# Optimization experiments

Measured on AMD Instinct MI355X. Metric: run time of the kernel, lower is better.

## Reference

```python
import jax, jax.numpy as jnp
import numpy as np

H, D, RPE_DIM, LAYERS = 8, 64, 64, 3
B, N = 8, 4096
EPS = 1e-8


def _srms(x):
    # SimpleRMSNorm: x / (||x||_2 / sqrt(d) + eps) == x / (rms(x) + eps)
    rms = jnp.sqrt(jnp.mean(x * x, axis=-1, keepdims=True))
    return x / (rms + EPS)


def _rpe(pos, w_in, b_in, w_layers, b_layers, w_out, b_out):
    # pos: [nf, 1] -> [nf, H*2*D]
    x = pos @ w_in + b_in
    for i in range(LAYERS):  # fixed small layer count
        x = jax.nn.relu(_srms(x)) @ w_layers[i] + b_layers[i]
    return jax.nn.relu(_srms(x)) @ w_out + b_out


def setup_inputs() -> dict:
    key = jax.random.key(0)
    ks = jax.random.split(key, 4)
    s = 0.02
    return {
        "x": jax.random.normal(ks[0], (B, H, N, D), jnp.float32),
        "w_in": jax.random.normal(ks[1], (1, RPE_DIM), jnp.float32) * s,
        "b_in": jnp.zeros((RPE_DIM,), jnp.float32),
        "w_layers": jax.random.normal(ks[2], (LAYERS, RPE_DIM, RPE_DIM), jnp.float32) * s,
        "b_layers": jnp.zeros((LAYERS, RPE_DIM), jnp.float32),
        "w_out": jax.random.normal(ks[3], (RPE_DIM, H * 2 * D), jnp.float32) * s,
        "b_out": jnp.zeros((H * 2 * D,), jnp.float32),
    }


def reference(x, w_in, b_in, w_layers, b_layers, w_out, b_out):
    # x: [b, h, n, d]; non-causal TnoFD with act_type='none' (identity act_fun)
    n = x.shape[-2]
    fft_size = 2 * n
    nf = fft_size // 2 + 1  # n + 1 frequencies
    pos = jnp.linspace(0.0, np.pi, nf, dtype=x.dtype).reshape(nf, 1)
    res = _rpe(pos, w_in, b_in, w_layers, b_layers, w_out, b_out)  # [nf, H*2D]
    # rearrange 'n (h d) -> h n d'
    res = res.reshape(nf, H, 2 * D).transpose(1, 0, 2)  # [H, nf, 2D]
    real, imag = res[..., :D], res[..., D:]
    imag = imag.at[:, 0, :].set(0.0).at[:, -1, :].set(0.0)
    a = real + 1j * imag  # [H, nf, D] complex filter
    y = jnp.fft.rfft(x, n=fft_size, axis=-2)  # [b, H, nf, D]
    out = jnp.fft.irfft(a * y, n=fft_size, axis=-2)[:, :, :n, :]
    return out.astype(x.dtype)
```

## Files before the change

### kernel.cpp

```cpp
#include <hip/hip_runtime.h>
#include <math.h>


#define PI_F 3.14159265358979323846f
#define TWO_PI_F 6.283185307179586f

__device__ __forceinline__ int dr4_3(int k) {
    return ((k & 3) << 4) | (k & 12) | ((k >> 4) & 3);
}

__global__ __launch_bounds__(512) void gen_tw_kernel(float2* __restrict__ tw4096,
                                                     float2* __restrict__ tw8192,
                                                     float2* __restrict__ e64)
{
    int idx = blockIdx.x * 512 + threadIdx.x;
    if (idx < 4096) {
        float s, c; __sincosf(TWO_PI_F * (float)idx * (1.0f / 4096.0f), &s, &c);
        tw4096[idx] = make_float2(c, s);
    } else if (idx < 8192) {
        int j = idx - 4096;
        float s, c; __sincosf(TWO_PI_F * (float)j * (1.0f / 8192.0f), &s, &c);
        tw8192[j] = make_float2(c, s);
    } else if (idx < 8256) {
        int j = idx - 8192;
        float s, c; __sincosf(TWO_PI_F * (float)j * (1.0f / 64.0f), &s, &c);
        e64[j] = make_float2(c, s);
    }
}

__device__ __forceinline__ void fft64_dif(float* re, float* im, int col, int ncol,
                                          int w, int nw, float sgn, bool act,
                                          const float2* e64s) {
    for (int S = 16, st = 1; S >= 1; S >>= 2, st <<= 2) {
        if (act) {
            for (int j = w; j < 16; j += nw) {
                const int q = j & (S - 1);
                const int u = q * st;
                const int i0 = ((j & ~(S - 1)) << 2) | q;
                const int p0 = i0 * ncol + col, p1 = (i0 + S) * ncol + col;
                const int p2 = (i0 + 2 * S) * ncol + col, p3 = (i0 + 3 * S) * ncol + col;
                float x0r = re[p0], x0i = im[p0], x1r = re[p1], x1i = im[p1];
                float x2r = re[p2], x2i = im[p2], x3r = re[p3], x3i = im[p3];
                float A0r = x0r + x2r, A0i = x0i + x2i, A1r = x0r - x2r, A1i = x0i - x2i;
                float A2r = x1r + x3r, A2i = x1i + x3i, A3r = x1r - x3r, A3i = x1i - x3i;
                float2 t1 = e64s[u], t2 = e64s[2 * u], t3 = e64s[3 * u];
                float c1 = t1.x, s1 = sgn * t1.y;
                float c2 = t2.x, s2 = sgn * t2.y;
                float c3 = t3.x, s3 = sgn * t3.y;
                re[p0] = A0r + A2r; im[p0] = A0i + A2i;
                float t1r = A1r - sgn * A3i, t1i = A1i + sgn * A3r;
                re[p1] = t1r * c1 - t1i * s1; im[p1] = t1r * s1 + t1i * c1;
                float t2r = A0r - A2r, t2i = A0i - A2i;
                re[p2] = t2r * c2 - t2i * s2; im[p2] = t2r * s2 + t2i * c2;
                float t3r = A1r + sgn * A3i, t3i = A1i - sgn * A3r;
                re[p3] = t3r * c3 - t3i * s3; im[p3] = t3r * s3 + t3i * c3;
            }
        }
        __syncthreads();
    }
}

__device__ __forceinline__ void fft64_dit(float* re, float* im, int col, int ncol,
                                          int w, int nw, float sgn, bool act,
                                          const float2* e64s) {
    for (int S = 1, st = 16; S <= 16; S <<= 2, st >>= 2) {
        if (act) {
            for (int j = w; j < 16; j += nw) {
                const int q = j & (S - 1);
                const int u = q * st;
                const int i0 = ((j & ~(S - 1)) << 2) | q;
                const int p0 = i0 * ncol + col, p1 = (i0 + S) * ncol + col;
                const int p2 = (i0 + 2 * S) * ncol + col, p3 = (i0 + 3 * S) * ncol + col;
                float y0r = re[p0], y0i = im[p0], y1r = re[p1], y1i = im[p1];
                float y2r = re[p2], y2i = im[p2], y3r = re[p3], y3i = im[p3];
                float2 t1 = e64s[u], t2 = e64s[2 * u], t3 = e64s[3 * u];
                float c1 = t1.x, s1 = sgn * t1.y;
                float c2 = t2.x, s2 = sgn * t2.y;
                float c3 = t3.x, s3 = sgn * t3.y;
                float x1r = y1r * c1 - y1i * s1, x1i = y1r * s1 + y1i * c1;
                float x2r = y2r * c2 - y2i * s2, x2i = y2r * s2 + y2i * c2;
                float x3r = y3r * c3 - y3i * s3, x3i = y3r * s3 + y3i * c3;
                float B0r = y0r + x2r, B0i = y0i + x2i, B1r = y0r - x2r, B1i = y0i - x2i;
                float B2r = x1r + x3r, B2i = x1i + x3i, B3r = x1r - x3r, B3i = x1i - x3i;
                re[p0] = B0r + B2r; im[p0] = B0i + B2i;
                re[p1] = B1r - sgn * B3i; im[p1] = B1i + sgn * B3r;
                re[p2] = B0r - B2r; im[p2] = B0i - B2i;
                re[p3] = B1r + sgn * B3i; im[p3] = B1i - sgn * B3r;
            }
        }
        __syncthreads();
    }
}

__global__ __launch_bounds__(256) void mlp_hidden_kernel(
    const float* __restrict__ w_in, const float* __restrict__ b_in,
    const float* __restrict__ w_layers, const float* __restrict__ b_layers,
    float* __restrict__ rbuf)
{
    const int lane = threadIdx.x & 63;
    const int k = blockIdx.x * 4 + (threadIdx.x >> 6);
    if (k > 4096) return;
    const float pos = PI_F * (float)k * (1.0f / 4096.0f);
    float xv = fmaf(pos, w_in[lane], b_in[lane]);
    for (int l = 0; l < 3; ++l) {
        float ss = xv * xv;
        #pragma unroll
        for (int o = 1; o < 64; o <<= 1) ss += __shfl_xor(ss, o, 64);
        float r = xv / (sqrtf(ss * (1.0f / 64.0f)) + 1e-8f);
        r = fmaxf(r, 0.0f);
        const float* W = w_layers + l * 4096;
        float a0 = 0.f, a1 = 0.f, a2 = 0.f, a3 = 0.f;
        for (int i = 0; i < 64; i += 4) {
            a0 = fmaf(__shfl(r, i, 64),     W[(i) * 64 + lane],     a0);
            a1 = fmaf(__shfl(r, i + 1, 64), W[(i + 1) * 64 + lane], a1);
            a2 = fmaf(__shfl(r, i + 2, 64), W[(i + 2) * 64 + lane], a2);
            a3 = fmaf(__shfl(r, i + 3, 64), W[(i + 3) * 64 + lane], a3);
        }
        xv = ((a0 + a1) + (a2 + a3)) + b_layers[l * 64 + lane];
    }
    float ss = xv * xv;
    #pragma unroll
    for (int o = 1; o < 64; o <<= 1) ss += __shfl_xor(ss, o, 64);
    float r = xv / (sqrtf(ss * (1.0f / 64.0f)) + 1e-8f);
    r = fmaxf(r, 0.0f);
    rbuf[(size_t)k * 64 + lane] = r;
}

__global__ __launch_bounds__(256) void mlp_out_kernel(
    const float* __restrict__ rbuf, const float* __restrict__ w_out,
    const float* __restrict__ b_out, float* __restrict__ res)
{
    __shared__ float rl[16 * 64];
    const int tid = threadIdx.x;
    const int nt = blockIdx.x, kt = blockIdx.y;
    for (int it = 0; it < 4; ++it) {
        int idx = it * 256 + tid;
        int row = idx >> 6, i = idx & 63;
        int k = kt * 16 + row;
        rl[idx] = (k <= 4096) ? rbuf[(size_t)k * 64 + i] : 0.0f;
    }
    __syncthreads();
    const int n = nt * 256 + tid;
    float acc[16];
    #pragma unroll
    for (int j = 0; j < 16; ++j) acc[j] = 0.0f;
    for (int i = 0; i < 64; ++i) {
        float wv = w_out[(size_t)i * 1024 + n];
        #pragma unroll
        for (int j = 0; j < 16; ++j)
            acc[j] = fmaf(rl[j * 64 + i], wv, acc[j]);
    }
    float bv = b_out[n];
    for (int j = 0; j < 16; ++j) {
        int k = kt * 16 + j;
        if (k <= 4096) res[(size_t)k * 1024 + n] = acc[j] + bv;
    }
}

__global__ __launch_bounds__(256) void fwd1_kernel(const float* __restrict__ x,
                                                   float2* __restrict__ Y,
                                                   const float2* __restrict__ tw4096,
                                                   const float2* __restrict__ e64g,
                                                   int slab_base)
{
    __shared__ float re[4096], im[4096];
    __shared__ float2 e64s[64];
    __shared__ float2 twA[64];
    const int tid = threadIdx.x;
    const int m0 = blockIdx.x, lslab = blockIdx.y;
    if (tid < 64) e64s[tid] = e64g[tid];
    else if (tid < 128) twA[tid - 64] = tw4096[m0 * (tid - 64)];
    const float* xs = x + (size_t)(slab_base + lslab) * 262144;
    for (int it = 0; it < 16; ++it) {
        int flat = it * 256 + tid;
        int m1 = flat >> 7, rr = (flat >> 6) & 1, d = flat & 63;
        float v = xs[(size_t)(128 * m1 + 2 * m0 + rr) * 64 + d];
        if (rr == 0) re[m1 * 64 + d] = v; else im[m1 * 64 + d] = v;
    }
    for (int i = 2048 + tid; i < 4096; i += 256) { re[i] = 0.0f; im[i] = 0.0f; }
    __syncthreads();
    const int d = tid & 63, w = tid >> 6;
    fft64_dif(re, im, d, 64, w, 4, -1.0f, true, e64s);
    float2* Ys = Y + (size_t)lslab * 262144 + (size_t)m0 * 64;
    for (int og = 0; og < 16; ++og) {
        int k1 = og * 4 + w;
        int slot = dr4_3(k1);
        float vr = re[slot * 64 + d], vi = im[slot * 64 + d];
        float2 t = twA[k1];
        float c = t.x, s = -t.y;
        Ys[(size_t)k1 * 4096 + d] = make_float2(vr * c - vi * s, vr * s + vi * c);
    }
}

__global__ __launch_bounds__(512) void midspec_kernel(float2* __restrict__ Y,
                                                      const float* __restrict__ res,
                                                      const float2* __restrict__ tw4096,
                                                      const float2* __restrict__ tw8192,
                                                      const float2* __restrict__ e64g,
                                                      int slab_base)
{
    __shared__ float re[8192], im[8192];
    __shared__ float2 e64s[64];
    __shared__ float2 twS[64];
    __shared__ float2 twB[128];
    const int tid = threadIdx.x;
    const int k1p = blockIdx.x;
    const int lslab = blockIdx.y;
    const int h = (slab_base + lslab) & 7;
    const bool pairwg = (k1p >= 1 && k1p <= 31);
    const int k1a = k1p;
    const int k1b = pairwg ? (64 - k1p) : k1p;
    const int NC = pairwg ? 128 : 64;

    if (tid < 64) e64s[tid] = e64g[tid];
    else if (tid < 128) twS[tid - 64] = tw8192[(tid - 64) * 64 + k1a];
    else if (tid < 256) {
        int i = tid - 128;
        int kk1 = (i < 64) ? k1a : k1b;
        twB[i] = tw4096[(i & 63) * kk1];
    }

    const float2* Pa = Y + (size_t)lslab * 262144 + (size_t)k1a * 4096;
    for (int it = 0; it < 4; ++it) {
        int idx4 = it * 512 + tid;
        const float4 v = ((const float4*)Pa)[idx4];
        int lin = idx4 * 2, m0 = lin >> 6, d = lin & 63;
        re[m0 * 128 + d] = v.x;     im[m0 * 128 + d] = v.y;
        re[m0 * 128 + d + 1] = v.z; im[m0 * 128 + d + 1] = v.w;
    }
    if (pairwg) {
        const float2* Pb = Y + (size_t)lslab * 262144 + (size_t)k1b * 4096;
        for (int it = 0; it < 4; ++it) {
            int idx4 = it * 512 + tid;
            const float4 v = ((const float4*)Pb)[idx4];
            int lin = idx4 * 2, m0 = lin >> 6, d = lin & 63;
            re[m0 * 128 + 64 + d] = v.x;     im[m0 * 128 + 64 + d] = v.y;
            re[m0 * 128 + 64 + d + 1] = v.z; im[m0 * 128 + 64 + d + 1] = v.w;
        }
    }
    __syncthreads();
    const int col = tid & 127, w8 = tid >> 7;
    fft64_dif(re, im, col, 128, w8, 4, -1.0f, col < NC, e64s);

    const int nit = pairwg ? 8 : 4;
    for (int it = 0; it < nit; ++it) {
        int item = it * 512 + tid;
        int k0 = item >> 6, d = item & 63;
        int c = h * 128 + d;
        if (k1p == 0 && k0 == 0) {
            float C0r = re[d], C0i = im[d];
            float X0 = C0r + C0i, XN = C0r - C0i;
            float a0 = res[c], aN = res[(size_t)4096 * 1024 + c];
            float S0 = a0 * X0, SN = aN * XN;
            re[d] = 0.5f * (S0 + SN); im[d] = 0.5f * (S0 - SN);
            int p2 = 2 * 128 + d;
            float Cr = re[p2], Ci = im[p2];
            float ar = res[(size_t)2048 * 1024 + c], ai = res[(size_t)2048 * 1024 + c + 64];
            float Sr = ar * Cr + ai * Ci, Si = ai * Cr - ar * Ci;
            re[p2] = Sr; im[p2] = -Si;
        } else {
            int k0p, coff;
            if (pairwg)          { k0p = 63 - k0;        coff = 64; }
            else if (k1p == 0)   { k0p = (64 - k0) & 63; coff = 0;  }
            else  { k0p = 63 - k0;        coff = 0;  }
            int sa = dr4_3(k0)  * 128 + d;
            int sb = dr4_3(k0p) * 128 + coff + d;
            int k  = k0 * 64 + k1a;
            int km = 4096 - k;
            float Ckr = re[sa], Cki = im[sa];
            float Cmr = re[sb], Cmi = im[sb];
            float Er = 0.5f * (Ckr + Cmr), Ei = 0.5f * (Cki - Cmi);
            float Dr = 0.5f * (Ckr - Cmr), Di = 0.5f * (Cki + Cmi);
            float Or = Di, Oi = -Dr;
            float2 tk = twS[k0];
            float cw = tk.x, sw = -tk.y;
            float Tr = Or * cw - Oi * sw, Ti = Or * sw + Oi * cw;
            float Xkr = Er + Tr, Xki = Ei + Ti;
            float Xmr = Er - Tr, Xmi = Ti - Ei;
            float akr = res[(size_t)k * 1024 + c],  aki = res[(size_t)k * 1024 + c + 64];
            float amr = res[(size_t)km * 1024 + c], ami = res[(size_t)km * 1024 + c + 64];
            float Skr = akr * Xkr - aki * Xki, Ski = akr * Xki + aki * Xkr;
            float Smr = amr * Xmr - ami * Xmi, Smi = amr * Xmi + ami * Xmr;
            float Epr = 0.5f * (Skr + Smr), Epi = 0.5f * (Ski - Smi);
            float Ddr = 0.5f * (Skr - Smr), Ddi = 0.5f * (Ski + Smi);
            float Opr = Ddr * cw + Ddi * sw, Opi = Ddi * cw - Ddr * sw;
            re[sa] = Epr - Opi; im[sa] = Epi + Opr;
            re[sb] = Epr + Opi; im[sb] = Opr - Epi;
        }
    }
    __syncthreads();
    fft64_dit(re, im, col, 128, w8, 4, +1.0f, col < NC, e64s);

    const int nit2 = pairwg ? 16 : 8;
    for (int it = 0; it < nit2; ++it) {
        int item = it * 512 + tid;
        int pl = item >> 12, rem = item & 4095;
        int m0 = rem >> 6, d = rem & 63;
        int cc = pl * 64 + d;
        int k1 = pl ? k1b : k1a;
        float vr = re[m0 * 128 + cc], vi = im[m0 * 128 + cc];
        float2 t = twB[pl * 64 + m0];
        float c2 = t.x, s = t.y;
        Y[(size_t)lslab * 262144 + (size_t)k1 * 4096 + (size_t)m0 * 64 + d] =
            make_float2(vr * c2 - vi * s, vr * s + vi * c2);
    }
}

__global__ __launch_bounds__(256) void inv2_kernel(const float2* __restrict__ Y,
                                                   float* __restrict__ out,
                                                   const float2* __restrict__ e64g,
                                                   int slab_base)
{
    __shared__ float re[4096], im[4096];
    __shared__ float2 e64s[64];
    const int tid = threadIdx.x;
    const int m0 = blockIdx.x, lslab = blockIdx.y;
    if (tid < 64) e64s[tid] = e64g[tid];
    const float2* Ys = Y + (size_t)lslab * 262144 + (size_t)m0 * 64;
    for (int it = 0; it < 8; ++it) {
        int idx4 = it * 256 + tid;
        int lin = idx4 * 2, k1 = lin >> 6, d = lin & 63;
        const float4 v = ((const float4*)Ys)[k1 * 2048 + (d >> 1)];
        re[k1 * 64 + d] = v.x;     im[k1 * 64 + d] = v.y;
        re[k1 * 64 + d + 1] = v.z; im[k1 * 64 + d + 1] = v.w;
    }
    __syncthreads();
    const int d = tid & 63, w = tid >> 6;
    fft64_dif(re, im, d, 64, w, 4, +1.0f, true, e64s);
    float* os = out + (size_t)(slab_base + lslab) * 262144;
    const float sc = 1.0f / 4096.0f;
    for (int it = 0; it < 16; ++it) {
        int flat = it * 256 + tid;
        int m1 = flat >> 7, rr = (flat >> 6) & 1, dd = flat & 63;
        int slot = dr4_3(m1);
        float v = rr ? im[slot * 64 + dd] : re[slot * 64 + dd];
        os[(size_t)(128 * m1 + 2 * m0 + rr) * 64 + dd] = v * sc;
    }
}

#define PADF(i) ((i) + ((i) >> 5))

__device__ __forceinline__ unsigned dr4_12(unsigned k) {
    unsigned rb = __brev(k) >> 20;
    return ((rb & 0x555u) << 1) | ((rb >> 1) & 0x555u);
}

__global__ __launch_bounds__(64) void rpe_mlp_kernel(
    const float* __restrict__ w_in, const float* __restrict__ b_in,
    const float* __restrict__ w_layers, const float* __restrict__ b_layers,
    const float* __restrict__ w_out, const float* __restrict__ b_out,
    float* __restrict__ res)
{
    const int k = blockIdx.x;
    const int lane = threadIdx.x;
    const float pos = PI_F * (float)k * (1.0f / 4096.0f);
    float xv = fmaf(pos, w_in[lane], b_in[lane]);
    for (int l = 0; l < 3; ++l) {
        float ss = xv * xv;
        #pragma unroll
        for (int o = 1; o < 64; o <<= 1) ss += __shfl_xor(ss, o, 64);
        float rms = sqrtf(ss * (1.0f / 64.0f));
        float r = xv / (rms + 1e-8f);
        r = r > 0.0f ? r : 0.0f;
        const float* W = w_layers + l * 64 * 64;
        float acc = b_layers[l * 64 + lane];
        for (int i = 0; i < 64; ++i)
            acc = fmaf(__shfl(r, i, 64), W[i * 64 + lane], acc);
        xv = acc;
    }
    float ss = xv * xv;
    #pragma unroll
    for (int o = 1; o < 64; o <<= 1) ss += __shfl_xor(ss, o, 64);
    float rms = sqrtf(ss * (1.0f / 64.0f));
    float r = xv / (rms + 1e-8f);
    r = r > 0.0f ? r : 0.0f;
    float acc[16];
    #pragma unroll
    for (int u = 0; u < 16; ++u) acc[u] = b_out[u * 64 + lane];
    for (int i = 0; i < 64; ++i) {
        float rv = __shfl(r, i, 64);
        const float* Wrow = w_out + i * 1024;
        #pragma unroll
        for (int u = 0; u < 16; ++u)
            acc[u] = fmaf(rv, Wrow[u * 64 + lane], acc[u]);
    }
    float* dst = res + (size_t)k * 1024;
    #pragma unroll
    for (int u = 0; u < 16; ++u) dst[u * 64 + lane] = acc[u];
}

__global__ __launch_bounds__(256) void fftconv_kernel(
    const float* __restrict__ x, const float* __restrict__ res,
    float* __restrict__ out)
{
    __shared__ float re[PADF(4095) + 1];
    __shared__ float im[PADF(4095) + 1];
    const int tid = threadIdx.x;
    const int blk = blockIdx.x;
    const int d = (blk >> 3) & 63;
    const int slab = (blk & 7) | ((blk >> 9) << 3);
    const int h = slab & 7;
    const size_t base = (size_t)slab * 4096 * 64 + (size_t)d;
    const float* xc = x + base;
    float* oc = out + base;
    const int c = h * 128 + d;
    for (int m = tid; m < 2048; m += 256) {
        re[PADF(m)] = xc[(size_t)(2 * m) * 64];
        im[PADF(m)] = xc[(size_t)(2 * m + 1) * 64];
    }
    for (int m = 2048 + tid; m < 4096; m += 256) { re[PADF(m)] = 0.0f; im[PADF(m)] = 0.0f; }
    __syncthreads();
    for (int S = 1024; S >= 1; S >>= 2) {
        const float ab = -TWO_PI_F / (float)(4 * S);
        for (int j = tid; j < 1024; j += 256) {
            const int q = j & (S - 1);
            const int i0 = ((j & ~(S - 1)) << 2) | q;
            const int p0 = PADF(i0), p1 = PADF(i0 + S), p2 = PADF(i0 + 2 * S), p3 = PADF(i0 + 3 * S);
            float x0r = re[p0], x0i = im[p0], x1r = re[p1], x1i = im[p1];
            float x2r = re[p2], x2i = im[p2], x3r = re[p3], x3i = im[p3];
            float A0r = x0r + x2r, A0i = x0i + x2i, A1r = x0r - x2r, A1i = x0i - x2i;
            float A2r = x1r + x3r, A2i = x1i + x3i, A3r = x1r - x3r, A3i = x1i - x3i;
            float s1, c1; __sincosf(ab * (float)q, &s1, &c1);
            float c2 = c1 * c1 - s1 * s1, s2 = 2.0f * c1 * s1;
            float c3 = c2 * c1 - s2 * s1, s3 = s2 * c1 + c2 * s1;
            re[p0] = A0r + A2r; im[p0] = A0i + A2i;
            float t1r = A1r + A3i, t1i = A1i - A3r;
            re[p1] = t1r * c1 - t1i * s1; im[p1] = t1r * s1 + t1i * c1;
            float t2r = A0r - A2r, t2i = A0i - A2i;
            re[p2] = t2r * c2 - t2i * s2; im[p2] = t2r * s2 + t2i * c2;
            float t3r = A1r - A3i, t3i = A1i + A3r;
            re[p3] = t3r * c3 - t3i * s3; im[p3] = t3r * s3 + t3i * c3;
        }
        __syncthreads();
    }
    for (int k = tid; k <= 2048; k += 256) {
        if (k == 0) {
            float C0r = re[0], C0i = im[0];
            float X0 = C0r + C0i, XN = C0r - C0i;
            float a0 = res[c], aN = res[(size_t)4096 * 1024 + c];
            float S0 = a0 * X0, SN = aN * XN;
            re[0] = 0.5f * (S0 + SN); im[0] = 0.5f * (S0 - SN);
        } else if (k == 2048) {
            const int p = PADF(2);
            float Cr = re[p], Ci = im[p];
            float ar = res[(size_t)2048 * 1024 + c], ai = res[(size_t)2048 * 1024 + c + 64];
            float Sr = ar * Cr + ai * Ci, Si = ai * Cr - ar * Ci;
            re[p] = Sr; im[p] = -Si;
        } else {
            const int pk = PADF((int)dr4_12((unsigned)k));
            const int pm = PADF((int)dr4_12((unsigned)(4096 - k)));
            float Ckr = re[pk], Cki = im[pk];
            float Cmr = re[pm], Cmi = im[pm];
            float Er = 0.5f * (Ckr + Cmr), Ei = 0.5f * (Cki - Cmi);
            float Dr = 0.5f * (Ckr - Cmr), Di = 0.5f * (Cki + Cmi);
            float Or = Di, Oi = -Dr;
            float sw, cw; __sincosf(-TWO_PI_F * (float)k * (1.0f / 8192.0f), &sw, &cw);
            float Tr = Or * cw - Oi * sw, Ti = Or * sw + Oi * cw;
            float Xkr = Er + Tr, Xki = Ei + Ti;
            float Xmr = Er - Tr, Xmi = Ti - Ei;
            float akr = res[(size_t)k * 1024 + c], aki = res[(size_t)k * 1024 + c + 64];
            float amr = res[(size_t)(4096 - k) * 1024 + c], ami = res[(size_t)(4096 - k) * 1024 + c + 64];
            float Skr = akr * Xkr - aki * Xki, Ski = akr * Xki + aki * Xkr;
            float Smr = amr * Xmr - ami * Xmi, Smi = amr * Xmi + ami * Xmr;
            float Epr = 0.5f * (Skr + Smr), Epi = 0.5f * (Ski - Smi);
            float Ddr = 0.5f * (Skr - Smr), Ddi = 0.5f * (Ski + Smi);
            float Opr = Ddr * cw + Ddi * sw, Opi = Ddi * cw - Ddr * sw;
            re[pk] = Epr - Opi; im[pk] = Epi + Opr;
            re[pm] = Epr + Opi; im[pm] = Opr - Epi;
        }
    }
    __syncthreads();
    for (int S = 1; S <= 1024; S <<= 2) {
        const float ab = TWO_PI_F / (float)(4 * S);
        for (int j = tid; j < 1024; j += 256) {
            const int q = j & (S - 1);
            const int i0 = ((j & ~(S - 1)) << 2) | q;
            const int p0 = PADF(i0), p1 = PADF(i0 + S), p2 = PADF(i0 + 2 * S), p3 = PADF(i0 + 3 * S);
            float y0r = re[p0], y0i = im[p0], y1r = re[p1], y1i = im[p1];
            float y2r = re[p2], y2i = im[p2], y3r = re[p3], y3i = im[p3];
            float s1, c1; __sincosf(ab * (float)q, &s1, &c1);
            float c2 = c1 * c1 - s1 * s1, s2 = 2.0f * c1 * s1;
            float c3 = c2 * c1 - s2 * s1, s3 = s2 * c1 + c2 * s1;
            float x1r = y1r * c1 - y1i * s1, x1i = y1r * s1 + y1i * c1;
            float x2r = y2r * c2 - y2i * s2, x2i = y2r * s2 + y2i * c2;
            float x3r = y3r * c3 - y3i * s3, x3i = y3r * s3 + y3i * c3;
            float B0r = y0r + x2r, B0i = y0i + x2i, B1r = y0r - x2r, B1i = y0i - x2i;
            float B2r = x1r + x3r, B2i = x1i + x3i, B3r = x1r - x3r, B3i = x1i - x3i;
            re[p0] = B0r + B2r; im[p0] = B0i + B2i;
            re[p1] = B1r - B3i; im[p1] = B1i + B3r;
            re[p2] = B0r - B2r; im[p2] = B0i - B2i;
            re[p3] = B1r + B3i; im[p3] = B1i - B3r;
        }
        __syncthreads();
    }
    const float sc = 1.0f / 4096.0f;
    for (int m = tid; m < 2048; m += 256) {
        oc[(size_t)(2 * m) * 64]     = re[PADF(m)] * sc;
        oc[(size_t)(2 * m + 1) * 64] = im[PADF(m)] * sc;
    }
}

extern "C" void kernel_launch(void* const* d_in, const int* in_sizes, int n_in,
                              void* d_out, int out_size, void* d_ws, size_t ws_size,
                              hipStream_t stream) {
    const float* x        = (const float*)d_in[0];
    const float* w_in     = (const float*)d_in[1];
    const float* b_in     = (const float*)d_in[2];
    const float* w_layers = (const float*)d_in[3];
    const float* b_layers = (const float*)d_in[4];
    const float* w_out    = (const float*)d_in[5];
    const float* b_out    = (const float*)d_in[6];
    float* out = (float*)d_out;
    float* wsf = (float*)d_ws;

    const size_t off_res    = 0;
    const size_t off_r      = 4195328;
    const size_t off_tw4096 = 4457536;
    const size_t off_tw8192 = off_tw4096 + 8192;
    const size_t off_e64    = off_tw8192 + 8192;
    const size_t off_Y      = off_e64 + 192;
    const size_t Y_PER_SLAB = 524288;

    float* res = wsf + off_res;
    const size_t avail_f = ws_size / 4;
    int nc = 0;
    if (avail_f > off_Y)
        nc = (int)((avail_f - off_Y) / Y_PER_SLAB);
    if (nc > 64) nc = 64;

    if (nc >= 1) {
        float2* tw4096 = (float2*)(wsf + off_tw4096);
        float2* tw8192 = (float2*)(wsf + off_tw8192);
        float2* e64    = (float2*)(wsf + off_e64);
        float2* Y      = (float2*)(wsf + off_Y);
        gen_tw_kernel<<<17, 512, 0, stream>>>(tw4096, tw8192, e64);
        mlp_hidden_kernel<<<1025, 256, 0, stream>>>(w_in, b_in, w_layers, b_layers,
                                                    wsf + off_r);
        mlp_out_kernel<<<dim3(4, 257), 256, 0, stream>>>(wsf + off_r, w_out, b_out, res);
        for (int s0 = 0; s0 < 64; s0 += nc) {
            int cur = (64 - s0 < nc) ? (64 - s0) : nc;
            fwd1_kernel<<<dim3(64, cur), 256, 0, stream>>>(x, Y, tw4096, e64, s0);
            midspec_kernel<<<dim3(33, cur), 512, 0, stream>>>(Y, res, tw4096, tw8192,
                                                              e64, s0);
            inv2_kernel<<<dim3(64, cur), 256, 0, stream>>>(Y, out, e64, s0);
        }
    } else {
        rpe_mlp_kernel<<<4097, 64, 0, stream>>>(w_in, b_in, w_layers, b_layers,
                                                w_out, b_out, res);
        fftconv_kernel<<<4096, 256, 0, stream>>>(x, res, out);
    }
}
```

Baseline: 279.9 us.

## Switch FFT-64 to register radix-8 passes with interleaved complex LDS and split midspec

Replaces the three radix-4 shared-memory passes of the 64-point FFT with two radix-8 passes computed in registers. This halves the number of LDS round trips and barriers per FFT. Shared storage changes from separate re/im arrays to interleaved float2, so loads and stores become vectorized. The midspec kernel is also split across two blocks per frequency pair, each handling half of the D columns with 256 threads and half the LDS, to raise occupancy. The trade-offs are higher register pressure, possible LDS bank conflicts on the strided float2 accesses, and changed index bookkeeping that correctness depends on.

```diff
diff --git a/kernel.cpp b/kernel.cpp
--- a/kernel.cpp
+++ b/kernel.cpp
@@ -5,8 +5,8 @@
 #define PI_F 3.14159265358979323846f
 #define TWO_PI_F 6.283185307179586f
 
-__device__ __forceinline__ int dr4_3(int k) {
-    return ((k & 3) << 4) | (k & 12) | ((k >> 4) & 3);
+__device__ __forceinline__ int r8(int k) {
+    return ((k & 7) << 3) | (k >> 3);
 }
 
 __global__ __launch_bounds__(512) void gen_tw_kernel(float2* __restrict__ tw4096,
@@ -28,68 +28,109 @@
     }
 }
 
-__device__ __forceinline__ void fft64_dif(float* re, float* im, int col, int ncol,
-                                          int w, int nw, float sgn, bool act,
-                                          const float2* e64s) {
-    for (int S = 16, st = 1; S >= 1; S >>= 2, st <<= 2) {
-        if (act) {
-            for (int j = w; j < 16; j += nw) {
-                const int q = j & (S - 1);
-                const int u = q * st;
-                const int i0 = ((j & ~(S - 1)) << 2) | q;
-                const int p0 = i0 * ncol + col, p1 = (i0 + S) * ncol + col;
-                const int p2 = (i0 + 2 * S) * ncol + col, p3 = (i0 + 3 * S) * ncol + col;
-                float x0r = re[p0], x0i = im[p0], x1r = re[p1], x1i = im[p1];
-                float x2r = re[p2], x2i = im[p2], x3r = re[p3], x3i = im[p3];
-                float A0r = x0r + x2r, A0i = x0i + x2i, A1r = x0r - x2r, A1i = x0i - x2i;
-                float A2r = x1r + x3r, A2i = x1i + x3i, A3r = x1r - x3r, A3i = x1i - x3i;
-                float2 t1 = e64s[u], t2 = e64s[2 * u], t3 = e64s[3 * u];
-                float c1 = t1.x, s1 = sgn * t1.y;
-                float c2 = t2.x, s2 = sgn * t2.y;
-                float c3 = t3.x, s3 = sgn * t3.y;
-                re[p0] = A0r + A2r; im[p0] = A0i + A2i;
-                float t1r = A1r - sgn * A3i, t1i = A1i + sgn * A3r;
-                re[p1] = t1r * c1 - t1i * s1; im[p1] = t1r * s1 + t1i * c1;
-                float t2r = A0r - A2r, t2i = A0i - A2i;
-                re[p2] = t2r * c2 - t2i * s2; im[p2] = t2r * s2 + t2i * c2;
-                float t3r = A1r + sgn * A3i, t3i = A1i - sgn * A3r;
-                re[p3] = t3r * c3 - t3i * s3; im[p3] = t3r * s3 + t3i * c3;
+__device__ __forceinline__ void fft8_regs(float2* v, float sgn) {
+    float t0r = v[0].x + v[4].x, t0i = v[0].y + v[4].y;
+    float t1r = v[0].x - v[4].x, t1i = v[0].y - v[4].y;
+    float t2r = v[2].x + v[6].x, t2i = v[2].y + v[6].y;
+    float t3r = v[2].x - v[6].x, t3i = v[2].y - v[6].y;
+    float e0r = t0r + t2r, e0i = t0i + t2i;
+    float e2r = t0r - t2r, e2i = t0i - t2i;
+    float e1r = t1r - sgn * t3i, e1i = t1i + sgn * t3r;
+    float e3r = t1r + sgn * t3i, e3i = t1i - sgn * t3r;
+    float u0r = v[1].x + v[5].x, u0i = v[1].y + v[5].y;
+    float u1r = v[1].x - v[5].x, u1i = v[1].y - v[5].y;
+    float u2r = v[3].x + v[7].x, u2i = v[3].y + v[7].y;
+    float u3r = v[3].x - v[7].x, u3i = v[3].y - v[7].y;
+    float o0r = u0r + u2r, o0i = u0i + u2i;
+    float o2r = u0r - u2r, o2i = u0i - u2i;
+    float o1r = u1r - sgn * u3i, o1i = u1i + sgn * u3r;
+    float o3r = u1r + sgn * u3i, o3i = u1i - sgn * u3r;
+    const float C = 0.70710678118654752f;
+    float w1r = C * (o1r - sgn * o1i), w1i = C * (o1i + sgn * o1r);
+    float w2r = -sgn * o2i,            w2i = sgn * o2r;
+    float w3r = -C * (o3r + sgn * o3i), w3i = C * (sgn * o3r - o3i);
+    v[0] = make_float2(e0r + o0r, e0i + o0i);
+    v[4] = make_float2(e0r - o0r, e0i - o0i);
+    v[1] = make_float2(e1r + w1r, e1i + w1i);
+    v[5] = make_float2(e1r - w1r, e1i - w1i);
+    v[2] = make_float2(e2r + w2r, e2i + w2i);
+    v[6] = make_float2(e2r - w2r, e2i - w2i);
+    v[3] = make_float2(e3r + w3r, e3i + w3i);
+    v[7] = make_float2(e3r - w3r, e3i - w3i);
+}
+
+__device__ __forceinline__ void fft64_dif(float2* zz, int col, int j0, float sgn,
+                                          bool act, const float2* e64s) {
+    if (act) {
+        #pragma unroll
+        for (int jj = 0; jj < 2; ++jj) {
+            const int j = j0 + jj * 4;
+            float2 v[8];
+            #pragma unroll
+            for (int r = 0; r < 8; ++r) v[r] = zz[(8 * r + j) * 64 + col];
+            fft8_regs(v, sgn);
+            #pragma unroll
+            for (int r = 1; r < 8; ++r) {
+                float2 t = e64s[j * r];
+                float c = t.x, s = sgn * t.y;
+                float vr = v[r].x, vi = v[r].y;
+                v[r] = make_float2(vr * c - vi * s, vr * s + vi * c);
             }
-        }
-        __syncthreads();
-    }
-}
-
-__device__ __forceinline__ void fft64_dit(float* re, float* im, int col, int ncol,
-                                          int w, int nw, float sgn, bool act,
-                                          const float2* e64s) {
-    for (int S = 1, st = 16; S <= 16; S <<= 2, st >>= 2) {
-        if (act) {
-            for (int j = w; j < 16; j += nw) {
-                const int q = j & (S - 1);
-                const int u = q * st;
-                const int i0 = ((j & ~(S - 1)) << 2) | q;
-                const int p0 = i0 * ncol + col, p1 = (i0 + S) * ncol + col;
-                const int p2 = (i0 + 2 * S) * ncol + col, p3 = (i0 + 3 * S) * ncol + col;
-                float y0r = re[p0], y0i = im[p0], y1r = re[p1], y1i = im[p1];
-                float y2r = re[p2], y2i = im[p2], y3r = re[p3], y3i = im[p3];
-                float2 t1 = e64s[u], t2 = e64s[2 * u], t3 = e64s[3 * u];
-                float c1 = t1.x, s1 = sgn * t1.y;
-                float c2 = t2.x, s2 = sgn * t2.y;
-                float c3 = t3.x, s3 = sgn * t3.y;
-                float x1r = y1r * c1 - y1i * s1, x1i = y1r * s1 + y1i * c1;
-                float x2r = y2r * c2 - y2i * s2, x2i = y2r * s2 + y2i * c2;
-                float x3r = y3r * c3 - y3i * s3, x3i = y3r * s3 + y3i * c3;
-                float B0r = y0r + x2r, B0i = y0i + x2i, B1r = y0r - x2r, B1i = y0i - x2i;
-                float B2r = x1r + x3r, B2i = x1i + x3i, B3r = x1r - x3r, B3i = x1i - x3i;
-                re[p0] = B0r + B2r; im[p0] = B0i + B2i;
-                re[p1] = B1r - sgn * B3i; im[p1] = B1i + sgn * B3r;
-                re[p2] = B0r - B2r; im[p2] = B0i - B2i;
-                re[p3] = B1r + sgn * B3i; im[p3] = B1i - sgn * B3r;
+            #pragma unroll
+            for (int r = 0; r < 8; ++r) zz[(8 * r + j) * 64 + col] = v[r];
+        }
+    }
+    __syncthreads();
+    if (act) {
+        #pragma unroll
+        for (int jj = 0; jj < 2; ++jj) {
+            const int j = j0 + jj * 4;
+            float2 v[8];
+            #pragma unroll
+            for (int r = 0; r < 8; ++r) v[r] = zz[(8 * j + r) * 64 + col];
+            fft8_regs(v, sgn);
+            #pragma unroll
+            for (int r = 0; r < 8; ++r) zz[(8 * j + r) * 64 + col] = v[r];
+        }
+    }
+    __syncthreads();
+}
+
+__device__ __forceinline__ void fft64_dit(float2* zz, int col, int j0, float sgn,
+                                          bool act, const float2* e64s) {
+    if (act) {
+        #pragma unroll
+        for (int jj = 0; jj < 2; ++jj) {
+            const int j = j0 + jj * 4;
+            float2 v[8];
+            #pragma unroll
+            for (int r = 0; r < 8; ++r) v[r] = zz[(8 * j + r) * 64 + col];
+            fft8_regs(v, sgn);
+            #pragma unroll
+            for (int r = 1; r < 8; ++r) {
+                float2 t = e64s[j * r];
+                float c = t.x, s = sgn * t.y;
+                float vr = v[r].x, vi = v[r].y;
+                v[r] = make_float2(vr * c - vi * s, vr * s + vi * c);
             }
-        }
-        __syncthreads();
-    }
+            #pragma unroll
+            for (int r = 0; r < 8; ++r) zz[(8 * j + r) * 64 + col] = v[r];
+        }
+    }
+    __syncthreads();
+    if (act) {
+        #pragma unroll
+        for (int jj = 0; jj < 2; ++jj) {
+            const int j = j0 + jj * 4;
+            float2 v[8];
+            #pragma unroll
+            for (int r = 0; r < 8; ++r) v[r] = zz[(8 * r + j) * 64 + col];
+            fft8_regs(v, sgn);
+            #pragma unroll
+            for (int r = 0; r < 8; ++r) zz[(8 * r + j) * 64 + col] = v[r];
+        }
+    }
+    __syncthreads();
 }
 
 __global__ __launch_bounds__(256) void mlp_hidden_kernel(
@@ -163,7 +204,7 @@
                                                    const float2* __restrict__ e64g,
                                                    int slab_base)
 {
-    __shared__ float re[4096], im[4096];
+    __shared__ float2 zz[4096];
     __shared__ float2 e64s[64];
     __shared__ float2 twA[64];
     const int tid = threadIdx.x;
@@ -172,105 +213,108 @@
     else if (tid < 128) twA[tid - 64] = tw4096[m0 * (tid - 64)];
     const float* xs = x + (size_t)(slab_base + lslab) * 262144;
     for (int it = 0; it < 16; ++it) {
-        int flat = it * 256 + tid;
-        int m1 = flat >> 7, rr = (flat >> 6) & 1, d = flat & 63;
-        float v = xs[(size_t)(128 * m1 + 2 * m0 + rr) * 64 + d];
-        if (rr == 0) re[m1 * 64 + d] = v; else im[m1 * 64 + d] = v;
-    }
-    for (int i = 2048 + tid; i < 4096; i += 256) { re[i] = 0.0f; im[i] = 0.0f; }
-    __syncthreads();
-    const int d = tid & 63, w = tid >> 6;
-    fft64_dif(re, im, d, 64, w, 4, -1.0f, true, e64s);
+        int slot = it * 256 + tid;
+        int m1 = slot >> 6, d = slot & 63;
+        if (m1 < 32) {
+            float vr = xs[(size_t)(128 * m1 + 2 * m0) * 64 + d];
+            float vi = xs[(size_t)(128 * m1 + 2 * m0 + 1) * 64 + d];
+            zz[slot] = make_float2(vr, vi);
+        } else {
+            zz[slot] = make_float2(0.0f, 0.0f);
+        }
+    }
+    __syncthreads();
+    const int col = tid & 63, j0 = tid >> 6;
+    fft64_dif(zz, col, j0, -1.0f, true, e64s);
     float2* Ys = Y + (size_t)lslab * 262144 + (size_t)m0 * 64;
     for (int og = 0; og < 16; ++og) {
-        int k1 = og * 4 + w;
-        int slot = dr4_3(k1);
-        float vr = re[slot * 64 + d], vi = im[slot * 64 + d];
+        int k1 = og * 4 + j0;
+        float2 v = zz[r8(k1) * 64 + col];
         float2 t = twA[k1];
         float c = t.x, s = -t.y;
-        Ys[(size_t)k1 * 4096 + d] = make_float2(vr * c - vi * s, vr * s + vi * c);
-    }
-}
-
-__global__ __launch_bounds__(512) void midspec_kernel(float2* __restrict__ Y,
+        Ys[(size_t)k1 * 4096 + col] = make_float2(v.x * c - v.y * s,
+                                                  v.x * s + v.y * c);
+    }
+}
+
+__global__ __launch_bounds__(256) void midspec_kernel(float2* __restrict__ Y,
                                                       const float* __restrict__ res,
                                                       const float2* __restrict__ tw4096,
                                                       const float2* __restrict__ tw8192,
                                                       const float2* __restrict__ e64g,
                                                       int slab_base)
 {
-    __shared__ float re[8192], im[8192];
+    __shared__ float2 zz[4096];
     __shared__ float2 e64s[64];
     __shared__ float2 twS[64];
     __shared__ float2 twB[128];
     const int tid = threadIdx.x;
-    const int k1p = blockIdx.x;
+    const int bx = blockIdx.x;
+    const int k1p = bx >> 1, dh = bx & 1;
     const int lslab = blockIdx.y;
     const int h = (slab_base + lslab) & 7;
     const bool pairwg = (k1p >= 1 && k1p <= 31);
     const int k1a = k1p;
     const int k1b = pairwg ? (64 - k1p) : k1p;
-    const int NC = pairwg ? 128 : 64;
+    const int NC = pairwg ? 64 : 32;
 
     if (tid < 64) e64s[tid] = e64g[tid];
     else if (tid < 128) twS[tid - 64] = tw8192[(tid - 64) * 64 + k1a];
-    else if (tid < 256) {
+    else {
         int i = tid - 128;
         int kk1 = (i < 64) ? k1a : k1b;
         twB[i] = tw4096[(i & 63) * kk1];
     }
 
-    const float2* Pa = Y + (size_t)lslab * 262144 + (size_t)k1a * 4096;
+    const float4* Pa4 = (const float4*)(Y + (size_t)lslab * 262144 + (size_t)k1a * 4096);
     for (int it = 0; it < 4; ++it) {
-        int idx4 = it * 512 + tid;
-        const float4 v = ((const float4*)Pa)[idx4];
-        int lin = idx4 * 2, m0 = lin >> 6, d = lin & 63;
-        re[m0 * 128 + d] = v.x;     im[m0 * 128 + d] = v.y;
-        re[m0 * 128 + d + 1] = v.z; im[m0 * 128 + d + 1] = v.w;
+        int idx4 = it * 256 + tid;
+        int m0 = idx4 >> 4, f = idx4 & 15;
+        float4 v = Pa4[m0 * 32 + 16 * dh + f];
+        *(float4*)&zz[m0 * 64 + 2 * f] = v;
     }
     if (pairwg) {
-        const float2* Pb = Y + (size_t)lslab * 262144 + (size_t)k1b * 4096;
+        const float4* Pb4 = (const float4*)(Y + (size_t)lslab * 262144 + (size_t)k1b * 4096);
         for (int it = 0; it < 4; ++it) {
-            int idx4 = it * 512 + tid;
-            const float4 v = ((const float4*)Pb)[idx4];
-            int lin = idx4 * 2, m0 = lin >> 6, d = lin & 63;
-            re[m0 * 128 + 64 + d] = v.x;     im[m0 * 128 + 64 + d] = v.y;
-            re[m0 * 128 + 64 + d + 1] = v.z; im[m0 * 128 + 64 + d + 1] = v.w;
-        }
-    }
-    __syncthreads();
-    const int col = tid & 127, w8 = tid >> 7;
-    fft64_dif(re, im, col, 128, w8, 4, -1.0f, col < NC, e64s);
+            int idx4 = it * 256 + tid;
+            int m0 = idx4 >> 4, f = idx4 & 15;
+            float4 v = Pb4[m0 * 32 + 16 * dh + f];
+            *(float4*)&zz[m0 * 64 + 32 + 2 * f] = v;
+        }
+    }
+    __syncthreads();
+    const int col = tid & 63, j0 = tid >> 6;
+    fft64_dif(zz, col, j0, -1.0f, col < NC, e64s);
 
     const int nit = pairwg ? 8 : 4;
     for (int it = 0; it < nit; ++it) {
-        int item = it * 512 + tid;
-        int k0 = item >> 6, d = item & 63;
-        int c = h * 128 + d;
+        int item = it * 256 + tid;
+        int k0 = item >> 5, dl = item & 31;
+        int c = h * 128 + 32 * dh + dl;
         if (k1p == 0 && k0 == 0) {
-            float C0r = re[d], C0i = im[d];
-            float X0 = C0r + C0i, XN = C0r - C0i;
+            float2 C0 = zz[dl];
+            float X0 = C0.x + C0.y, XN = C0.x - C0.y;
             float a0 = res[c], aN = res[(size_t)4096 * 1024 + c];
             float S0 = a0 * X0, SN = aN * XN;
-            re[d] = 0.5f * (S0 + SN); im[d] = 0.5f * (S0 - SN);
-            int p2 = 2 * 128 + d;
-            float Cr = re[p2], Ci = im[p2];
+            zz[dl] = make_float2(0.5f * (S0 + SN), 0.5f * (S0 - SN));
+            int p2 = 4 * 64 + dl;
+            float2 Cq = zz[p2];
             float ar = res[(size_t)2048 * 1024 + c], ai = res[(size_t)2048 * 1024 + c + 64];
-            float Sr = ar * Cr + ai * Ci, Si = ai * Cr - ar * Ci;
-            re[p2] = Sr; im[p2] = -Si;
+            float Sr = ar * Cq.x + ai * Cq.y;
+            float Si = ai * Cq.x - ar * Cq.y;
+            zz[p2] = make_float2(Sr, -Si);
         } else {
             int k0p, coff;
-            if (pairwg)          { k0p = 63 - k0;        coff = 64; }
+            if (pairwg)          { k0p = 63 - k0;        coff = 32; }
             else if (k1p == 0)   { k0p = (64 - k0) & 63; coff = 0;  }
             else  { k0p = 63 - k0;        coff = 0;  }
-            int sa = dr4_3(k0)  * 128 + d;
-            int sb = dr4_3(k0p) * 128 + coff + d;
+            int sa = r8(k0)  * 64 + dl;
+            int sb = r8(k0p) * 64 + coff + dl;
             int k  = k0 * 64 + k1a;
             int km = 4096 - k;
-            float Ckr = re[sa], Cki = im[sa];
-            float Cmr = re[sb], Cmi = im[sb];
-            float Er = 0.5f * (Ckr + Cmr), Ei = 0.5f * (Cki - Cmi);
-            float Dr = 0.5f * (Ckr - Cmr), Di = 0.5f * (Cki + Cmi);
+            float2 Ck = zz[sa], Cm = zz[sb];
+            float Er = 0.5f * (Ck.x + Cm.x), Ei = 0.5f * (Ck.y - Cm.y);
+            float Dr = 0.5f * (Ck.x - Cm.x), Di = 0.5f * (Ck.y + Cm.y);
             float Or = Di, Oi = -Dr;
             float2 tk = twS[k0];
             float cw = tk.x, sw = -tk.y;
@@ -284,25 +328,24 @@
             float Epr = 0.5f * (Skr + Smr), Epi = 0.5f * (Ski - Smi);
             float Ddr = 0.5f * (Skr - Smr), Ddi = 0.5f * (Ski + Smi);
             float Opr = Ddr * cw + Ddi * sw, Opi = Ddi * cw - Ddr * sw;
-            re[sa] = Epr - Opi; im[sa] = Epi + Opr;
-            re[sb] = Epr + Opi; im[sb] = Opr - Epi;
-        }
-    }
-    __syncthreads();
-    fft64_dit(re, im, col, 128, w8, 4, +1.0f, col < NC, e64s);
+            zz[sa] = make_float2(Epr - Opi, Epi + Opr);
+            zz[sb] = make_float2(Epr + Opi, Opr - Epi);
+        }
+    }
+    __syncthreads();
+    fft64_dit(zz, col, j0, +1.0f, col < NC, e64s);
 
     const int nit2 = pairwg ? 16 : 8;
     for (int it = 0; it < nit2; ++it) {
-        int item = it * 512 + tid;
-        int pl = item >> 12, rem = item & 4095;
-        int m0 = rem >> 6, d = rem & 63;
-        int cc = pl * 64 + d;
+        int item = it * 256 + tid;
+        int pl = item >> 11, rem = item & 2047;
+        int m0 = rem >> 5, dl = rem & 31;
         int k1 = pl ? k1b : k1a;
-        float vr = re[m0 * 128 + cc], vi = im[m0 * 128 + cc];
+        float2 v = zz[m0 * 64 + pl * 32 + dl];
         float2 t = twB[pl * 64 + m0];
         float c2 = t.x, s = t.y;
-        Y[(size_t)lslab * 262144 + (size_t)k1 * 4096 + (size_t)m0 * 64 + d] =
-            make_float2(vr * c2 - vi * s, vr * s + vi * c2);
+        Y[(size_t)lslab * 262144 + (size_t)k1 * 4096 + (size_t)m0 * 64 + 32 * dh + dl] =
+            make_float2(v.x * c2 - v.y * s, v.x * s + v.y * c2);
     }
 }
 
@@ -311,30 +354,30 @@
                                                    const float2* __restrict__ e64g,
                                                    int slab_base)
 {
-    __shared__ float re[4096], im[4096];
+    __shared__ float2 zz[4096];
     __shared__ float2 e64s[64];
     const int tid = threadIdx.x;
     const int m0 = blockIdx.x, lslab = blockIdx.y;
     if (tid < 64) e64s[tid] = e64g[tid];
     const float2* Ys = Y + (size_t)lslab * 262144 + (size_t)m0 * 64;
+    const float4* Ys4 = (const float4*)Ys;
     for (int it = 0; it < 8; ++it) {
         int idx4 = it * 256 + tid;
-        int lin = idx4 * 2, k1 = lin >> 6, d = lin & 63;
-        const float4 v = ((const float4*)Ys)[k1 * 2048 + (d >> 1)];
-        re[k1 * 64 + d] = v.x;     im[k1 * 64 + d] = v.y;
-        re[k1 * 64 + d + 1] = v.z; im[k1 * 64 + d + 1] = v.w;
-    }
-    __syncthreads();
-    const int d = tid & 63, w = tid >> 6;
-    fft64_dif(re, im, d, 64, w, 4, +1.0f, true, e64s);
+        int k1 = idx4 >> 5, f = idx4 & 31;
+        float4 v = Ys4[k1 * 2048 + f];
+        *(float4*)&zz[k1 * 64 + 2 * f] = v;
+    }
+    __syncthreads();
+    const int col = tid & 63, j0 = tid >> 6;
+    fft64_dif(zz, col, j0, +1.0f, true, e64s);
     float* os = out + (size_t)(slab_base + lslab) * 262144;
     const float sc = 1.0f / 4096.0f;
-    for (int it = 0; it < 16; ++it) {
-        int flat = it * 256 + tid;
-        int m1 = flat >> 7, rr = (flat >> 6) & 1, dd = flat & 63;
-        int slot = dr4_3(m1);
-        float v = rr ? im[slot * 64 + dd] : re[slot * 64 + dd];
-        os[(size_t)(128 * m1 + 2 * m0 + rr) * 64 + dd] = v * sc;
+    for (int it = 0; it < 8; ++it) {
+        int slot = it * 256 + tid;
+        int m1 = slot >> 6, d = slot & 63;
+        float2 v = zz[r8(m1) * 64 + d];
+        os[(size_t)(128 * m1 + 2 * m0) * 64 + d]     = v.x * sc;
+        os[(size_t)(128 * m1 + 2 * m0 + 1) * 64 + d] = v.y * sc;
     }
 }
 
@@ -540,7 +583,7 @@
         for (int s0 = 0; s0 < 64; s0 += nc) {
             int cur = (64 - s0 < nc) ? (64 - s0) : nc;
             fwd1_kernel<<<dim3(64, cur), 256, 0, stream>>>(x, Y, tw4096, e64, s0);
-            midspec_kernel<<<dim3(33, cur), 512, 0, stream>>>(Y, res, tw4096, tw8192,
+            midspec_kernel<<<dim3(66, cur), 256, 0, stream>>>(Y, res, tw4096, tw8192,
                                                               e64, s0);
             inv2_kernel<<<dim3(64, cur), 256, 0, stream>>>(Y, out, e64, s0);
         }
```

Result: faster. 274.2 us (-2.0%).
